# Kernel tuning notes

Hardware: AMD Instinct MI355X
Metric: run time of the kernel (lower is better)

## Reference

```python
import jax, jax.numpy as jnp
import numpy as np

B, R, IN, OUT = 32, 4, 1024, 1024
PI_MIX, SIGMA1, SIGMA2 = 0.5, 1.0, 0.1


def setup_inputs() -> dict:
    key = jax.random.key(0)
    ks = jax.random.split(key, 7)
    return {
        "x": jax.random.normal(ks[0], (B, IN), dtype=jnp.float32),
        "mu": jax.random.normal(ks[1], (IN, OUT), dtype=jnp.float32),
        "ro": jax.random.normal(ks[2], (IN, OUT), dtype=jnp.float32),
        "mu_bias": jax.random.normal(ks[3], (1, OUT), dtype=jnp.float32),
        "ro_bias": jax.random.normal(ks[4], (1, OUT), dtype=jnp.float32),
        "eps": jax.random.normal(ks[5], (B, R, IN, OUT), dtype=jnp.float32),
        "eps_bias": jax.random.normal(ks[6], (B, R, OUT), dtype=jnp.float32),
    }


def _gaussian(v, m, s):
    # pdf, clamped like the torch code
    bell = jnp.exp(-(v - m) ** 2 / (2.0 * s ** 2)) / (jnp.sqrt(2.0 * jnp.pi) * s)
    return jnp.clip(bell, 1e-10, 10.0)


def _mixture(v):
    return PI_MIX * _gaussian(v, 0.0, SIGMA1) + (1.0 - PI_MIX) * _gaussian(v, 0.0, SIGMA2)


def reference(x, mu, ro, mu_bias, ro_bias, eps, eps_bias):
    sigma = jnp.log1p(jnp.exp(ro))              # softplus, (IN, OUT)
    sigma_b = jnp.log1p(jnp.exp(ro_bias))       # (1, OUT)
    weights = eps * sigma + mu                  # (B, R, IN, OUT)
    bias = eps_bias * sigma_b + mu_bias         # (B, R, OUT)
    denom = x.shape[0] * R
    log_prior = (jnp.log(_mixture(weights)).sum() + jnp.log(_mixture(bias)).sum()) / denom
    log_p_weights = (jnp.log(_gaussian(weights, mu, sigma)).sum()
                     + jnp.log(_gaussian(bias, mu_bias, sigma_b)).sum()) / denom
    # out[b, r] = x[b] @ weights[b, r] + bias[b, r]; mean over r
    out = (jnp.einsum('bi,brio->bro', x, weights) + bias).mean(axis=1)  # (B, OUT)
    return out, log_prior, log_p_weights
```

## Files before the change

### kernel.cpp

```cpp
#include <hip/hip_runtime.h>
#include <math.h>

#define B_    32
#define R_    4
#define IN_   1024
#define OUT_  1024
#define S_    16
#define CHUNK (IN_ / S_)
#define NPRE  ((size_t)IN_ * OUT_ + OUT_)

#define C_HALF_LOG_2PI 0.9189385332046727f
#define INV_SQRT_2PI   0.3989422804014327f
#define INV_SQRT_2PI_S 3.9894228040143270f
#define LOG_MIN       -23.025850929940457f
#define LOG_MAX        2.3025850929940460f

__device__ __forceinline__ float softplus_f(float x) {
    return fmaxf(x, 0.0f) + log1pf(__expf(-fabsf(x)));
}

__global__ void init_kernel(float* __restrict__ out) {
    int idx = blockIdx.x * 256 + threadIdx.x;
    if (idx < B_ * OUT_ + 2) out[idx] = 0.0f;
}

__global__ void precomp_kernel(const float* __restrict__ ro,
                               const float* __restrict__ ro_bias,
                               float* __restrict__ sig,
                               float* __restrict__ lpb) {
    size_t idx = (size_t)blockIdx.x * 256 + threadIdx.x;
    if (idx >= NPRE) return;
    float rv = (idx < (size_t)IN_ * OUT_) ? ro[idx] : ro_bias[idx - (size_t)IN_ * OUT_];
    float sg = softplus_f(rv);
    sig[idx] = sg;
    lpb[idx] = -C_HALF_LOG_2PI - __logf(sg);
}

#define PROC(E, M, SG, LB, ACC)                                              \
    {                                                                        \
        float w  = fmaf((E), (SG), (M));                                     \
        (ACC)    = fmaf(xv, w, (ACC));                                       \
        float t  = -0.5f * w * w;                                            \
        float g1 = fmaxf(__expf(t)          * INV_SQRT_2PI,   1e-10f);       \
        float g2 = fmaxf(__expf(100.0f * t) * INV_SQRT_2PI_S, 1e-10f);       \
        smix += __logf(0.5f * (g1 + g2));                                    \
        float lw = fmaf((E) * (E), -0.5f, (LB));                             \
        slpw += fminf(fmaxf(lw, LOG_MIN), LOG_MAX);                          \
    }

template <bool USE_WS>
__global__ __launch_bounds__(256)
void main_kernel(const float* __restrict__ x,
                 const float* __restrict__ mu,
                 const float* __restrict__ ro,
                 const float* __restrict__ mu_bias,
                 const float* __restrict__ ro_bias,
                 const float* __restrict__ eps,
                 const float* __restrict__ eps_bias,
                 const float* __restrict__ sig_ws,
                 const float* __restrict__ lpb_ws,
                 float* __restrict__ out) {
    const int tid = threadIdx.x;
    const int bid = blockIdx.x;
    const int s   = bid & (S_ - 1);
    const int r   = (bid >> 4) & (R_ - 1);
    const int b   = bid >> 6;
    const int i0  = s * CHUNK;

    __shared__ float xs[CHUNK];
    if (tid < CHUNK) xs[tid] = x[b * IN_ + i0 + tid];
    __syncthreads();

    const size_t row0 = ((size_t)(b * R_ + r) * IN_ + i0) * OUT_;
    const float4* eps4 = (const float4*)(eps + row0) + tid;
    const float4* mu4  = (const float4*)(mu + (size_t)i0 * OUT_) + tid;
    const float4* ro4  = (const float4*)(ro + (size_t)i0 * OUT_) + tid;
    const float4* sig4 = USE_WS ? (const float4*)(sig_ws + (size_t)i0 * OUT_) + tid : nullptr;
    const float4* lpb4 = USE_WS ? (const float4*)(lpb_ws + (size_t)i0 * OUT_) + tid : nullptr;

    float4 acc = {0.f, 0.f, 0.f, 0.f};
    float smix = 0.f, slpw = 0.f;

    for (int ii = 0; ii < CHUNK; ++ii) {
        const int stride = ii * (OUT_ / 4);
        float  xv = xs[ii];
        float4 e  = eps4[stride];
        float4 m  = mu4[stride];
        float4 sg, lb;
        if (USE_WS) {
            sg = sig4[stride];
            lb = lpb4[stride];
        } else {
            float4 rr = ro4[stride];
            sg.x = softplus_f(rr.x); lb.x = -C_HALF_LOG_2PI - __logf(sg.x);
            sg.y = softplus_f(rr.y); lb.y = -C_HALF_LOG_2PI - __logf(sg.y);
            sg.z = softplus_f(rr.z); lb.z = -C_HALF_LOG_2PI - __logf(sg.z);
            sg.w = softplus_f(rr.w); lb.w = -C_HALF_LOG_2PI - __logf(sg.w);
        }
        PROC(e.x, m.x, sg.x, lb.x, acc.x);
        PROC(e.y, m.y, sg.y, lb.y, acc.y);
        PROC(e.z, m.z, sg.z, lb.z, acc.z);
        PROC(e.w, m.w, sg.w, lb.w, acc.w);
    }

    if (s == 0) {
        float4 eb = *((const float4*)(eps_bias + (size_t)(b * R_ + r) * OUT_) + tid);
        float4 mb = *((const float4*)mu_bias + tid);
        float4 sgb, lbb;
        if (USE_WS) {
            sgb = *((const float4*)(sig_ws + (size_t)IN_ * OUT_) + tid);
            lbb = *((const float4*)(lpb_ws + (size_t)IN_ * OUT_) + tid);
        } else {
            float4 rb = *((const float4*)ro_bias + tid);
            sgb.x = softplus_f(rb.x); lbb.x = -C_HALF_LOG_2PI - __logf(sgb.x);
            sgb.y = softplus_f(rb.y); lbb.y = -C_HALF_LOG_2PI - __logf(sgb.y);
            sgb.z = softplus_f(rb.z); lbb.z = -C_HALF_LOG_2PI - __logf(sgb.z);
            sgb.w = softplus_f(rb.w); lbb.w = -C_HALF_LOG_2PI - __logf(sgb.w);
        }
        float xv = 1.0f;
        PROC(eb.x, mb.x, sgb.x, lbb.x, acc.x);
        PROC(eb.y, mb.y, sgb.y, lbb.y, acc.y);
        PROC(eb.z, mb.z, sgb.z, lbb.z, acc.z);
        PROC(eb.w, mb.w, sgb.w, lbb.w, acc.w);
    }

    float* outp = out + (size_t)b * OUT_ + tid * 4;
    atomicAdd(outp + 0, acc.x * 0.25f);
    atomicAdd(outp + 1, acc.y * 0.25f);
    atomicAdd(outp + 2, acc.z * 0.25f);
    atomicAdd(outp + 3, acc.w * 0.25f);

    for (int off = 32; off > 0; off >>= 1) {
        smix += __shfl_down(smix, off, 64);
        slpw += __shfl_down(slpw, off, 64);
    }
    __shared__ float red[8];
    const int wave = tid >> 6, lane = tid & 63;
    if (lane == 0) { red[wave] = smix; red[4 + wave] = slpw; }
    __syncthreads();
    if (tid == 0) {
        float sm = red[0] + red[1] + red[2] + red[3];
        float sl = red[4] + red[5] + red[6] + red[7];
        atomicAdd(out + B_ * OUT_ + 0, sm * (1.0f / 128.0f));
        atomicAdd(out + B_ * OUT_ + 1, sl * (1.0f / 128.0f));
    }
}

extern "C" void kernel_launch(void* const* d_in, const int* in_sizes, int n_in,
                              void* d_out, int out_size, void* d_ws, size_t ws_size,
                              hipStream_t stream) {
    const float* x       = (const float*)d_in[0];
    const float* mu      = (const float*)d_in[1];
    const float* ro      = (const float*)d_in[2];
    const float* mu_bias = (const float*)d_in[3];
    const float* ro_bias = (const float*)d_in[4];
    const float* eps     = (const float*)d_in[5];
    const float* eps_b   = (const float*)d_in[6];
    float* out = (float*)d_out;

    const bool use_ws = ws_size >= 2 * NPRE * sizeof(float);
    float* sig_ws = (float*)d_ws;
    float* lpb_ws = sig_ws + NPRE;

    init_kernel<<<(B_ * OUT_ + 2 + 255) / 256, 256, 0, stream>>>(out);

    if (use_ws) {
        precomp_kernel<<<(int)((NPRE + 255) / 256), 256, 0, stream>>>(ro, ro_bias, sig_ws, lpb_ws);
        main_kernel<true><<<B_ * R_ * S_, 256, 0, stream>>>(
            x, mu, ro, mu_bias, ro_bias, eps, eps_b, sig_ws, lpb_ws, out);
    } else {
        main_kernel<false><<<B_ * R_ * S_, 256, 0, stream>>>(
            x, mu, ro, mu_bias, ro_bias, eps, eps_b, nullptr, nullptr, out);
    }
}
```

Before: 759.7 us.

## Process all R samples per block to reuse mu/sigma loads; fold init into precompute

Each block now loops over all four R samples for a given batch and input chunk. The mu and sigma rows are loaded once and reused across the samples, and the log-sigma term is recomputed in registers instead of being read from a second workspace array. The chunk count grows to keep the same number of blocks, the separate output-zeroing kernel is merged into the precompute kernel, and the workspace shrinks to a single array. The change trades extra __logf work per element for less memory traffic on mu/sigma/lpb and one fewer kernel launch.

```diff
diff --git a/kernel.cpp b/kernel.cpp
--- a/kernel.cpp
+++ b/kernel.cpp
@@ -5,7 +5,7 @@
 #define R_    4
 #define IN_   1024
 #define OUT_  1024
-#define S_    16
+#define S_    64
 #define CHUNK (IN_ / S_)
 #define NPRE  ((size_t)IN_ * OUT_ + OUT_)
 
@@ -27,13 +27,12 @@
 __global__ void precomp_kernel(const float* __restrict__ ro,
                                const float* __restrict__ ro_bias,
                                float* __restrict__ sig,
-                               float* __restrict__ lpb) {
+                               float* __restrict__ out) {
     size_t idx = (size_t)blockIdx.x * 256 + threadIdx.x;
+    if (idx < B_ * OUT_ + 2) out[idx] = 0.0f;
     if (idx >= NPRE) return;
     float rv = (idx < (size_t)IN_ * OUT_) ? ro[idx] : ro_bias[idx - (size_t)IN_ * OUT_];
-    float sg = softplus_f(rv);
-    sig[idx] = sg;
-    lpb[idx] = -C_HALF_LOG_2PI - __logf(sg);
+    sig[idx] = softplus_f(rv);
 }
 
 #define PROC(E, M, SG, LB, ACC)                                              \
@@ -58,12 +57,10 @@
                  const float* __restrict__ eps,
                  const float* __restrict__ eps_bias,
                  const float* __restrict__ sig_ws,
-                 const float* __restrict__ lpb_ws,
                  float* __restrict__ out) {
     const int tid = threadIdx.x;
     const int bid = blockIdx.x;
     const int s   = bid & (S_ - 1);
-    const int r   = (bid >> 4) & (R_ - 1);
     const int b   = bid >> 6;
     const int i0  = s * CHUNK;
 
@@ -71,57 +68,71 @@
     if (tid < CHUNK) xs[tid] = x[b * IN_ + i0 + tid];
     __syncthreads();
 
-    const size_t row0 = ((size_t)(b * R_ + r) * IN_ + i0) * OUT_;
-    const float4* eps4 = (const float4*)(eps + row0) + tid;
     const float4* mu4  = (const float4*)(mu + (size_t)i0 * OUT_) + tid;
-    const float4* ro4  = (const float4*)(ro + (size_t)i0 * OUT_) + tid;
     const float4* sig4 = USE_WS ? (const float4*)(sig_ws + (size_t)i0 * OUT_) + tid : nullptr;
-    const float4* lpb4 = USE_WS ? (const float4*)(lpb_ws + (size_t)i0 * OUT_) + tid : nullptr;
+    const float4* ro4  = USE_WS ? nullptr : (const float4*)(ro + (size_t)i0 * OUT_) + tid;
+
+    const float4* e4[R_];
+#pragma unroll
+    for (int r = 0; r < R_; ++r)
+        e4[r] = (const float4*)(eps + ((size_t)(b * R_ + r) * IN_ + i0) * OUT_) + tid;
 
     float4 acc = {0.f, 0.f, 0.f, 0.f};
     float smix = 0.f, slpw = 0.f;
 
     for (int ii = 0; ii < CHUNK; ++ii) {
         const int stride = ii * (OUT_ / 4);
-        float  xv = xs[ii];
-        float4 e  = eps4[stride];
-        float4 m  = mu4[stride];
+        const float xv = xs[ii];
+        float4 m = mu4[stride];
         float4 sg, lb;
         if (USE_WS) {
             sg = sig4[stride];
-            lb = lpb4[stride];
         } else {
             float4 rr = ro4[stride];
-            sg.x = softplus_f(rr.x); lb.x = -C_HALF_LOG_2PI - __logf(sg.x);
-            sg.y = softplus_f(rr.y); lb.y = -C_HALF_LOG_2PI - __logf(sg.y);
-            sg.z = softplus_f(rr.z); lb.z = -C_HALF_LOG_2PI - __logf(sg.z);
-            sg.w = softplus_f(rr.w); lb.w = -C_HALF_LOG_2PI - __logf(sg.w);
+            sg.x = softplus_f(rr.x);
+            sg.y = softplus_f(rr.y);
+            sg.z = softplus_f(rr.z);
+            sg.w = softplus_f(rr.w);
         }
-        PROC(e.x, m.x, sg.x, lb.x, acc.x);
-        PROC(e.y, m.y, sg.y, lb.y, acc.y);
-        PROC(e.z, m.z, sg.z, lb.z, acc.z);
-        PROC(e.w, m.w, sg.w, lb.w, acc.w);
+        lb.x = -C_HALF_LOG_2PI - __logf(sg.x);
+        lb.y = -C_HALF_LOG_2PI - __logf(sg.y);
+        lb.z = -C_HALF_LOG_2PI - __logf(sg.z);
+        lb.w = -C_HALF_LOG_2PI - __logf(sg.w);
+#pragma unroll
+        for (int r = 0; r < R_; ++r) {
+            float4 e = e4[r][stride];
+            PROC(e.x, m.x, sg.x, lb.x, acc.x);
+            PROC(e.y, m.y, sg.y, lb.y, acc.y);
+            PROC(e.z, m.z, sg.z, lb.z, acc.z);
+            PROC(e.w, m.w, sg.w, lb.w, acc.w);
+        }
     }
 
     if (s == 0) {
-        float4 eb = *((const float4*)(eps_bias + (size_t)(b * R_ + r) * OUT_) + tid);
-        float4 mb = *((const float4*)mu_bias + tid);
+        float4 mb = ((const float4*)mu_bias)[tid];
         float4 sgb, lbb;
         if (USE_WS) {
-            sgb = *((const float4*)(sig_ws + (size_t)IN_ * OUT_) + tid);
-            lbb = *((const float4*)(lpb_ws + (size_t)IN_ * OUT_) + tid);
+            sgb = ((const float4*)(sig_ws + (size_t)IN_ * OUT_))[tid];
         } else {
-            float4 rb = *((const float4*)ro_bias + tid);
-            sgb.x = softplus_f(rb.x); lbb.x = -C_HALF_LOG_2PI - __logf(sgb.x);
-            sgb.y = softplus_f(rb.y); lbb.y = -C_HALF_LOG_2PI - __logf(sgb.y);
-            sgb.z = softplus_f(rb.z); lbb.z = -C_HALF_LOG_2PI - __logf(sgb.z);
-            sgb.w = softplus_f(rb.w); lbb.w = -C_HALF_LOG_2PI - __logf(sgb.w);
+            float4 rb = ((const float4*)ro_bias)[tid];
+            sgb.x = softplus_f(rb.x);
+            sgb.y = softplus_f(rb.y);
+            sgb.z = softplus_f(rb.z);
+            sgb.w = softplus_f(rb.w);
         }
-        float xv = 1.0f;
-        PROC(eb.x, mb.x, sgb.x, lbb.x, acc.x);
-        PROC(eb.y, mb.y, sgb.y, lbb.y, acc.y);
-        PROC(eb.z, mb.z, sgb.z, lbb.z, acc.z);
-        PROC(eb.w, mb.w, sgb.w, lbb.w, acc.w);
+        lbb.x = -C_HALF_LOG_2PI - __logf(sgb.x);
+        lbb.y = -C_HALF_LOG_2PI - __logf(sgb.y);
+        lbb.z = -C_HALF_LOG_2PI - __logf(sgb.z);
+        lbb.w = -C_HALF_LOG_2PI - __logf(sgb.w);
+        const float xv = 1.0f;
+#pragma unroll
+        for (int r = 0; r < R_; ++r) {
+            float4 eb = ((const float4*)(eps_bias + (size_t)(b * R_ + r) * OUT_))[tid];
+            PROC(eb.x, mb.x, sgb.x, lbb.x, acc.x);
+            PROC(eb.y, mb.y, sgb.y, lbb.y, acc.y);
+            PROC(eb.z, mb.z, sgb.z, lbb.z, acc.z);
+            PROC(eb.w, mb.w, sgb.w, lbb.w, acc.w);
+        }
     }
 
     float* outp = out + (size_t)b * OUT_ + tid * 4;
@@ -158,18 +169,16 @@
     const float* eps_b   = (const float*)d_in[6];
     float* out = (float*)d_out;
 
-    const bool use_ws = ws_size >= 2 * NPRE * sizeof(float);
+    const bool use_ws = ws_size >= NPRE * sizeof(float);
     float* sig_ws = (float*)d_ws;
-    float* lpb_ws = sig_ws + NPRE;
-
-    init_kernel<<<(B_ * OUT_ + 2 + 255) / 256, 256, 0, stream>>>(out);
 
     if (use_ws) {
-        precomp_kernel<<<(int)((NPRE + 255) / 256), 256, 0, stream>>>(ro, ro_bias, sig_ws, lpb_ws);
-        main_kernel<true><<<B_ * R_ * S_, 256, 0, stream>>>(
-            x, mu, ro, mu_bias, ro_bias, eps, eps_b, sig_ws, lpb_ws, out);
+        precomp_kernel<<<(int)((NPRE + 255) / 256), 256, 0, stream>>>(ro, ro_bias, sig_ws, out);
+        main_kernel<true><<<B_ * S_, 256, 0, stream>>>(
+            x, mu, ro, mu_bias, ro_bias, eps, eps_b, sig_ws, out);
     } else {
-        main_kernel<false><<<B_ * R_ * S_, 256, 0, stream>>>(
-            x, mu, ro, mu_bias, ro_bias, eps, eps_b, nullptr, nullptr, out);
+        init_kernel<<<(B_ * OUT_ + 2 + 255) / 256, 256, 0, stream>>>(out);
+        main_kernel<false><<<B_ * S_, 256, 0, stream>>>(
+            x, mu, ro, mu_bias, ro_bias, eps, eps_b, nullptr, out);
     }
 }
```

New measurement: 736.7 us. 1.03x faster.
